# Kernel optimization log

Hardware: AMD Instinct MI355X
Metric: run time of the kernel (lower is better)

## Reference

```python
import jax, jax.numpy as jnp
import numpy as np

NUM_HEADS = 8

def setup_inputs() -> dict:
    key = jax.random.key(0)
    ks = jax.random.split(key, 5)
    b, c, h, w = 8, 512, 32, 32
    sd = 1.0 / np.sqrt(c)
    x = jax.random.normal(ks[0], (b, c, h, w), dtype=jnp.float32)
    Wq = jax.random.normal(ks[1], (c, c), dtype=jnp.float32) * sd
    Wk = jax.random.normal(ks[2], (c, c), dtype=jnp.float32) * sd
    Wv = jax.random.normal(ks[3], (c, c), dtype=jnp.float32) * sd
    Wo = jax.random.normal(ks[4], (c, c), dtype=jnp.float32) * sd
    z = jnp.zeros((c,), dtype=jnp.float32)
    return {"x": x, "Wq": Wq, "bq": z, "Wk": Wk, "bk": z, "Wv": Wv, "bv": z, "Wo": Wo, "bo": z}

def reference(x, Wq, bq, Wk, bk, Wv, bv, Wo, bo):
    b, c, h, w = x.shape
    nh = NUM_HEADS
    hd = c // nh
    # [b, c, h, w] -> [b, h*w, c]
    xr = jnp.transpose(x, (0, 2, 3, 1)).reshape(b, h * w, c)
    def proj(W, bias):
        y = xr @ W.T + bias
        return y.reshape(b, h * w, nh, hd)
    q = proj(Wq, bq)  # [b, s, nh, hd]
    k = proj(Wk, bk)
    v = proj(Wv, bv)
    scale = 1.0 / np.sqrt(hd)
    att = jnp.einsum("bsnd,btnd->bnst", q, k) * scale  # [b, nh, s, s]
    att = jax.nn.softmax(att, axis=-1)
    # dropout is identity in eval mode
    out = jnp.einsum("bnst,btnd->bsnd", att, v).reshape(b, h, w, c)
    out = out @ Wo.T + bo  # [b, h, w, c]
    return out
```

## Files before the change

### kernel.cpp

```cpp
#include <hip/hip_runtime.h>

typedef _Float16 half_t;
typedef _Float16 half2v __attribute__((ext_vector_type(2)));
typedef _Float16 half8 __attribute__((ext_vector_type(8)));
typedef float f32x4 __attribute__((ext_vector_type(4)));

static_assert(sizeof(half8) == 16, "half8 must be 16B");

__device__ inline half8 make_h8(unsigned long lo, unsigned long hi) {
  union { half8 v; unsigned long u[2]; } x;
  x.u[0] = lo; x.u[1] = hi;
  return x.v;
}

__device__ inline float fast_exp2(float x) {
#if __has_builtin(__builtin_amdgcn_exp2f)
  return __builtin_amdgcn_exp2f(x);
#else
  return exp2f(x);
#endif
}

__device__ inline half2v cvt_pk_f16(float lo, float hi) {
  return __builtin_bit_cast(half2v, __builtin_amdgcn_cvt_pkrtz(lo, hi));
}

__device__ inline void gload_lds16(const void* g, void* l) {
  __builtin_amdgcn_global_load_lds(
      (const __attribute__((address_space(1))) unsigned int*)g,
      (__attribute__((address_space(3))) unsigned int*)l, 16, 0, 0);
}

__global__ void prep_kernel(const float* __restrict__ x,
                            const float* __restrict__ w0, const float* __restrict__ w1,
                            const float* __restrict__ w2, const float* __restrict__ w3,
                            half_t* __restrict__ xr, half_t* __restrict__ wout) {
  if (blockIdx.z < 8) {
    __shared__ float t[32][33];
    const int b = blockIdx.z;
    const int c0 = blockIdx.y * 32;
    const int s0 = blockIdx.x * 32;
    const int tx = threadIdx.x, ty = threadIdx.y;
    const float* xp = x + ((size_t)b * 512 + c0) * 1024 + s0;
#pragma unroll
    for (int r = 0; r < 4; r++) {
      const int cl = ty + 8 * r;
      t[cl][tx] = xp[(size_t)cl * 1024 + tx];
    }
    __syncthreads();
    half_t* op = xr + ((size_t)b * 1024 + s0) * 512 + c0;
#pragma unroll
    for (int r = 0; r < 4; r++) {
      const int sl = ty + 8 * r;
      op[(size_t)sl * 512 + tx] = (half_t)t[tx][sl];
    }
  } else {
    const int f = blockIdx.x + 32 * blockIdx.y;
    const int tid = threadIdx.x + 32 * threadIdx.y;
    const int base = (f * 256 + tid) * 2;
#pragma unroll
    for (int r = 0; r < 2; r++) {
      const int i = base + r;
      const int mz = i >> 16;
      const float* src = (mz == 0) ? w0 : (mz == 1) ? w1 : (mz == 2) ? w2 : w3;
      const float4 v = ((const float4*)src)[i & 65535];
      union { half_t e[4]; unsigned long u; } st;
      st.e[0] = (half_t)v.x; st.e[1] = (half_t)v.y;
      st.e[2] = (half_t)v.z; st.e[3] = (half_t)v.w;
      *(unsigned long*)(wout + (size_t)i * 4) = st.u;
    }
  }
}

template <int MODE, int BM>
__global__ __launch_bounds__(256, 2) void gemm_kernel(
    const half_t* __restrict__ A, const half_t* __restrict__ Wall,
    const float* __restrict__ b0, const float* __restrict__ b1,
    const float* __restrict__ b2, half_t* __restrict__ qkv,
    float* __restrict__ fout) {
  constexpr int K = 512;
  constexpr int IREP = BM / 32;
  __shared__ alignas(16) half_t lA[BM * 64];
  __shared__ alignas(16) half_t lB[128 * 64];

  int bx, by, bz;
  {
    const int flat = blockIdx.x + gridDim.x * (blockIdx.y + gridDim.y * blockIdx.z);
    const int xcd = flat & 7;
    const int r = flat >> 3;
    if (MODE == 0) {
      bx = r & 3; bz = (r >> 2) % 3; by = (r / 12) * 8 + xcd;
    } else {
      bx = r & 3; bz = 0; by = (r >> 2) * 8 + xcd;
    }
  }

  const int z = bz;
  const half_t* W = Wall + (size_t)z * K * 512;
  const float* bias = (MODE == 1) ? b0 : (z == 0 ? b0 : (z == 1 ? b1 : b2));

  const int tid = threadIdx.x;
  const int lane = tid & 63;
  const int wid = tid >> 6;
  const int wm = wid >> 1, wn = wid & 1;
  const int g = lane >> 4, r16 = lane & 15;
  const int m0 = by * BM, n0 = bx * 128;

  f32x4 acc[IREP][4];
#pragma unroll
  for (int i = 0; i < IREP; i++)
#pragma unroll
    for (int j = 0; j < 4; j++) acc[i][j] = (f32x4){0.f, 0.f, 0.f, 0.f};

  for (int k0 = 0; k0 < K; k0 += 64) {
#pragma unroll
    for (int t = 0; t < BM / 32; t++) {
      const int o = (t * 256 + tid) * 16;
      const int row = o >> 7;
      const int kbs = (o & 127) ^ ((row & 7) << 4);
      gload_lds16((const char*)(A + (size_t)(m0 + row) * K + k0) + kbs, (char*)lA + o);
    }
#pragma unroll
    for (int t = 0; t < 4; t++) {
      const int o = (t * 256 + tid) * 16;
      const int row = o >> 7;
      const int kbs = (o & 127) ^ ((row & 7) << 4);
      gload_lds16((const char*)(W + (size_t)(n0 + row) * K + k0) + kbs, (char*)lB + o);
    }
    __syncthreads();
#pragma unroll
    for (int kk = 0; kk < 2; kk++) {
      half8 af[IREP], bf[4];
#pragma unroll
      for (int i = 0; i < IREP; i++) {
        const int row = wm * (BM / 2) + i * 16 + r16;
        const int sw = (row & 7) << 4;
        const char* p = (const char*)lA + row * 128;
        af[i] = make_h8(*(const unsigned long*)(p + ((kk * 64 + g * 8) ^ sw)),
                        *(const unsigned long*)(p + ((kk * 64 + 32 + g * 8) ^ sw)));
      }
#pragma unroll
      for (int j = 0; j < 4; j++) {
        const int row = wn * 64 + j * 16 + r16;
        const int sw = (row & 7) << 4;
        const char* p = (const char*)lB + row * 128;
        bf[j] = make_h8(*(const unsigned long*)(p + ((kk * 64 + g * 8) ^ sw)),
                        *(const unsigned long*)(p + ((kk * 64 + 32 + g * 8) ^ sw)));
      }
#pragma unroll
      for (int i = 0; i < IREP; i++)
#pragma unroll
        for (int j = 0; j < 4; j++)
          acc[i][j] = __builtin_amdgcn_mfma_f32_16x16x32_f16(af[i], bf[j], acc[i][j], 0, 0, 0);
    }
    __syncthreads();
  }

  half_t* dst = (MODE == 0) ? (qkv + (size_t)z * 4194304) : (half_t*)nullptr;
  const float scale = (MODE == 0 && z == 0) ? 0.18033688011112042f : 1.0f;
#pragma unroll
  for (int i = 0; i < IREP; i++) {
#pragma unroll
    for (int j = 0; j < 4; j++) {
      const int n = n0 + wn * 64 + j * 16 + r16;
      const float bvv = bias[n];
      const int mb = m0 + wm * (BM / 2) + i * 16 + g * 4;
      if (MODE == 0 && z == 2) {
        const int bb = mb >> 10, s0v = mb & 1023, hh = n >> 6, d = n & 63;
        const int kvb = s0v & 31;
        const int sp0 = (s0v & ~31) | ((((kvb & 15) >> 2) << 3) + ((kvb >> 4) << 2));
        half_t* dp = dst + (size_t)(bb * 8 + hh) * 65536 + ((size_t)d << 10) + sp0;
        union { half_t e[4]; unsigned long u; } st;
#pragma unroll
        for (int rr = 0; rr < 4; rr++) st.e[rr] = (half_t)(acc[i][j][rr] + bvv);
        *(unsigned long*)dp = st.u;
      } else {
#pragma unroll
        for (int rr = 0; rr < 4; rr++) {
          const int m = mb + rr;
          const float v = (acc[i][j][rr] + bvv) * scale;
          if (MODE == 0) {
            const int bb = m >> 10, s = m & 1023, hh = n >> 6, d = n & 63;
            dst[(((size_t)(bb * 8 + hh) * 1024 + s) << 6) + d] = (half_t)v;
          } else {
            fout[(size_t)m * 512 + n] = v;
          }
        }
      }
    }
  }
}


__device__ inline half8 lds_frag128(const half_t* l, int row, int cb) {
  const char* p = (const char*)l + row * 128 + (cb ^ ((row & 7) << 4));
  return *(const half8*)p;
}

__global__ __launch_bounds__(256) void attn_kernel(
    const half_t* __restrict__ Q, const half_t* __restrict__ Kh,
    const half_t* __restrict__ V, half_t* __restrict__ O) {
  __shared__ alignas(16) half_t lK[2][64 * 64];
  __shared__ alignas(16) half_t lV[2][64 * 64];

  const int tid = threadIdx.x;
  const int lane = tid & 63;
  const int w = tid >> 6;
  const int flat = blockIdx.x + (blockIdx.y << 3);
  const int xcd = flat & 7;
  const int tt = flat >> 3;
  const int qch = tt & 7;
  const int bh = ((tt >> 3) << 3) | xcd;
  const int b = bh >> 3, h = bh & 7;
  const int g = lane >> 4, r16 = lane & 15;
  const size_t base = (size_t)bh * 65536;
  const half_t* Qp = Q + base;
  const half_t* Kp = Kh + base;
  const half_t* Vt = V + base;
  const int q0 = qch * 128 + w * 32;

  half8 qf[2][2];
#pragma unroll
  for (int qt = 0; qt < 2; qt++) {
    const half_t* qrow = Qp + (size_t)(q0 + qt * 16 + r16) * 64 + g * 8;
    qf[qt][0] = *(const half8*)(qrow);
    qf[qt][1] = *(const half8*)(qrow + 32);
  }

  f32x4 acc[2][4];
#pragma unroll
  for (int qt = 0; qt < 2; qt++)
#pragma unroll
    for (int i = 0; i < 4; i++) acc[qt][i] = (f32x4){0.f, 0.f, 0.f, 0.f};
  float lsum[2] = {0.f, 0.f};

  auto stage = [&](int kv0, int bufi) {
    half_t* lk = lK[bufi];
    half_t* lv = lV[bufi];
    const char* ksrc = (const char*)(Kp + (size_t)kv0 * 64);
    const char* vsrc = (const char*)Vt + (size_t)kv0 * 2;
#pragma unroll
    for (int i = 0; i < 2; i++) {
      const int o = i * 4096 + tid * 16;
      const int row = o >> 7;
      const int cs = (o & 127) ^ ((row & 7) << 4);
      gload_lds16(ksrc + row * 128 + cs, (char*)lk + o);
      gload_lds16(vsrc + row * 2048 + cs, (char*)lv + o);
    }
  };

  stage(0, 0);
  __syncthreads();

  int buf = 0;
  for (int kv0 = 0; kv0 < 1024; kv0 += 64) {
    if (kv0 + 64 < 1024) stage(kv0 + 64, buf ^ 1);
    const half_t* lk = lK[buf];
    const half_t* lv = lV[buf];
#pragma unroll
    for (int sub = 0; sub < 2; sub++) {
      half8 kf0 = lds_frag128(lk, sub * 32 + r16, g * 16);
      half8 kf1 = lds_frag128(lk, sub * 32 + r16, 64 + g * 16);
      half8 kf2 = lds_frag128(lk, sub * 32 + 16 + r16, g * 16);
      half8 kf3 = lds_frag128(lk, sub * 32 + 16 + r16, 64 + g * 16);
      half8 vf[4];
#pragma unroll
      for (int dt = 0; dt < 4; dt++)
        vf[dt] = lds_frag128(lv, dt * 16 + r16, sub * 64 + g * 16);

#pragma unroll
      for (int qt = 0; qt < 2; qt++) {
        f32x4 s0 = {0.f, 0.f, 0.f, 0.f}, s1 = {0.f, 0.f, 0.f, 0.f};
        __builtin_amdgcn_s_setprio(1);
        s0 = __builtin_amdgcn_mfma_f32_16x16x32_f16(kf0, qf[qt][0], s0, 0, 0, 0);
        s0 = __builtin_amdgcn_mfma_f32_16x16x32_f16(kf1, qf[qt][1], s0, 0, 0, 0);
        s1 = __builtin_amdgcn_mfma_f32_16x16x32_f16(kf2, qf[qt][0], s1, 0, 0, 0);
        s1 = __builtin_amdgcn_mfma_f32_16x16x32_f16(kf3, qf[qt][1], s1, 0, 0, 0);
        __builtin_amdgcn_s_setprio(0);

        float p[8];
#pragma unroll
        for (int i = 0; i < 4; i++) { p[i] = fast_exp2(s0[i]); p[4 + i] = fast_exp2(s1[i]); }
        lsum[qt] += ((p[0] + p[1]) + (p[2] + p[3])) + ((p[4] + p[5]) + (p[6] + p[7]));

        union { half8 v; half2v h2[4]; } pu;
#pragma unroll
        for (int i = 0; i < 4; i++)
          pu.h2[i] = cvt_pk_f16(p[2 * i], p[2 * i + 1]);
        __builtin_amdgcn_s_setprio(1);
#pragma unroll
        for (int dt = 0; dt < 4; dt++)
          acc[qt][dt] = __builtin_amdgcn_mfma_f32_16x16x32_f16(vf[dt], pu.v, acc[qt][dt], 0, 0, 0);
        __builtin_amdgcn_s_setprio(0);
      }
    }
    __syncthreads();
    buf ^= 1;
  }

#pragma unroll
  for (int qt = 0; qt < 2; qt++) {
    float l = lsum[qt];
    l += __shfl_xor(l, 16);
    l += __shfl_xor(l, 32);
    const float inv = 1.f / l;
    half_t* orow = O + ((size_t)b * 1024 + q0 + qt * 16 + r16) * 512 + h * 64;
#pragma unroll
    for (int dt = 0; dt < 4; dt++) {
      union { half_t e[4]; unsigned long u; } st;
#pragma unroll
      for (int rr = 0; rr < 4; rr++) st.e[rr] = (half_t)(acc[qt][dt][rr] * inv);
      *(unsigned long*)(orow + dt * 16 + g * 4) = st.u;
    }
  }
}

extern "C" void kernel_launch(void* const* d_in, const int* in_sizes, int n_in,
                              void* d_out, int out_size, void* d_ws, size_t ws_size,
                              hipStream_t stream) {
  if (ws_size < 44040192u) return;
  const float* x  = (const float*)d_in[0];
  const float* Wq = (const float*)d_in[1];
  const float* bq = (const float*)d_in[2];
  const float* Wk = (const float*)d_in[3];
  const float* bk = (const float*)d_in[4];
  const float* Wv = (const float*)d_in[5];
  const float* bv = (const float*)d_in[6];
  const float* Wo = (const float*)d_in[7];
  const float* bo = (const float*)d_in[8];
  char* ws = (char*)d_ws;
  half_t* xr = (half_t*)(ws + 0);
  half_t* W4 = (half_t*)(ws + 8388608);
  half_t* Qb = (half_t*)(ws + 10485760);
  half_t* AO = (half_t*)(ws + 35651584);
  float* out = (float*)d_out;

  prep_kernel<<<dim3(32, 16, 9), dim3(32, 8), 0, stream>>>(x, Wq, Wk, Wv, Wo, xr, W4);
  gemm_kernel<0, 128><<<dim3(4, 64, 3), 256, 0, stream>>>(xr, W4, bq, bk, bv, Qb, nullptr);
  attn_kernel<<<dim3(8, 64), 256, 0, stream>>>(Qb, Qb + 4194304, Qb + 8388608, AO);
  gemm_kernel<1, 64><<<dim3(4, 128, 1), 256, 0, stream>>>(AO, W4 + 786432, bo, nullptr, nullptr,
                                                          nullptr, out);
}
```

Baseline: 70.55 us.

## Double KV tile to 128 and batch QK/PV MFMAs across query tiles

```diff
diff --git a/kernel.cpp b/kernel.cpp
--- a/kernel.cpp
+++ b/kernel.cpp
@@ -197,11 +197,16 @@
   return *(const half8*)p;
 }
 
+__device__ inline half8 lds_frag256(const half_t* l, int row, int cb) {
+  const char* p = (const char*)l + row * 256 + (cb ^ ((row & 7) << 4));
+  return *(const half8*)p;
+}
+
 __global__ __launch_bounds__(256) void attn_kernel(
     const half_t* __restrict__ Q, const half_t* __restrict__ Kh,
     const half_t* __restrict__ V, half_t* __restrict__ O) {
-  __shared__ alignas(16) half_t lK[2][64 * 64];
-  __shared__ alignas(16) half_t lV[2][64 * 64];
+  __shared__ alignas(16) half_t lK[2][128 * 64];
+  __shared__ alignas(16) half_t lV[2][64 * 128];
 
   const int tid = threadIdx.x;
   const int lane = tid & 63;
@@ -240,12 +245,14 @@
     const char* ksrc = (const char*)(Kp + (size_t)kv0 * 64);
     const char* vsrc = (const char*)Vt + (size_t)kv0 * 2;
 #pragma unroll
-    for (int i = 0; i < 2; i++) {
+    for (int i = 0; i < 4; i++) {
       const int o = i * 4096 + tid * 16;
-      const int row = o >> 7;
-      const int cs = (o & 127) ^ ((row & 7) << 4);
-      gload_lds16(ksrc + row * 128 + cs, (char*)lk + o);
-      gload_lds16(vsrc + row * 2048 + cs, (char*)lv + o);
+      const int krow = o >> 7;
+      const int kcs = (o & 127) ^ ((krow & 7) << 4);
+      gload_lds16(ksrc + krow * 128 + kcs, (char*)lk + o);
+      const int vrow = o >> 8;
+      const int vcs = (o & 255) ^ ((vrow & 7) << 4);
+      gload_lds16(vsrc + vrow * 2048 + vcs, (char*)lv + o);
     }
   };
 
@@ -253,12 +260,12 @@
   __syncthreads();
 
   int buf = 0;
-  for (int kv0 = 0; kv0 < 1024; kv0 += 64) {
-    if (kv0 + 64 < 1024) stage(kv0 + 64, buf ^ 1);
+  for (int kv0 = 0; kv0 < 1024; kv0 += 128) {
+    if (kv0 + 128 < 1024) stage(kv0 + 128, buf ^ 1);
     const half_t* lk = lK[buf];
     const half_t* lv = lV[buf];
 #pragma unroll
-    for (int sub = 0; sub < 2; sub++) {
+    for (int sub = 0; sub < 4; sub++) {
       half8 kf0 = lds_frag128(lk, sub * 32 + r16, g * 16);
       half8 kf1 = lds_frag128(lk, sub * 32 + r16, 64 + g * 16);
       half8 kf2 = lds_frag128(lk, sub * 32 + 16 + r16, g * 16);
@@ -266,33 +273,43 @@
       half8 vf[4];
 #pragma unroll
       for (int dt = 0; dt < 4; dt++)
-        vf[dt] = lds_frag128(lv, dt * 16 + r16, sub * 64 + g * 16);
-
+        vf[dt] = lds_frag256(lv, dt * 16 + r16, sub * 64 + g * 16);
+
+      f32x4 s[2][2];
+      __builtin_amdgcn_s_setprio(1);
 #pragma unroll
       for (int qt = 0; qt < 2; qt++) {
-        f32x4 s0 = {0.f, 0.f, 0.f, 0.f}, s1 = {0.f, 0.f, 0.f, 0.f};
-        __builtin_amdgcn_s_setprio(1);
-        s0 = __builtin_amdgcn_mfma_f32_16x16x32_f16(kf0, qf[qt][0], s0, 0, 0, 0);
-        s0 = __builtin_amdgcn_mfma_f32_16x16x32_f16(kf1, qf[qt][1], s0, 0, 0, 0);
-        s1 = __builtin_amdgcn_mfma_f32_16x16x32_f16(kf2, qf[qt][0], s1, 0, 0, 0);
-        s1 = __builtin_amdgcn_mfma_f32_16x16x32_f16(kf3, qf[qt][1], s1, 0, 0, 0);
-        __builtin_amdgcn_s_setprio(0);
-
+        s[qt][0] = (f32x4){0.f, 0.f, 0.f, 0.f};
+        s[qt][1] = (f32x4){0.f, 0.f, 0.f, 0.f};
+        s[qt][0] = __builtin_amdgcn_mfma_f32_16x16x32_f16(kf0, qf[qt][0], s[qt][0], 0, 0, 0);
+        s[qt][0] = __builtin_amdgcn_mfma_f32_16x16x32_f16(kf1, qf[qt][1], s[qt][0], 0, 0, 0);
+        s[qt][1] = __builtin_amdgcn_mfma_f32_16x16x32_f16(kf2, qf[qt][0], s[qt][1], 0, 0, 0);
+        s[qt][1] = __builtin_amdgcn_mfma_f32_16x16x32_f16(kf3, qf[qt][1], s[qt][1], 0, 0, 0);
+      }
+      __builtin_amdgcn_s_setprio(0);
+
+      union { half8 v; half2v h2[4]; } pu[2];
+#pragma unroll
+      for (int qt = 0; qt < 2; qt++) {
         float p[8];
 #pragma unroll
-        for (int i = 0; i < 4; i++) { p[i] = fast_exp2(s0[i]); p[4 + i] = fast_exp2(s1[i]); }
+        for (int i = 0; i < 4; i++) {
+          p[i] = fast_exp2(s[qt][0][i]);
+          p[4 + i] = fast_exp2(s[qt][1][i]);
+        }
         lsum[qt] += ((p[0] + p[1]) + (p[2] + p[3])) + ((p[4] + p[5]) + (p[6] + p[7]));
-
-        union { half8 v; half2v h2[4]; } pu;
 #pragma unroll
         for (int i = 0; i < 4; i++)
-          pu.h2[i] = cvt_pk_f16(p[2 * i], p[2 * i + 1]);
-        __builtin_amdgcn_s_setprio(1);
+          pu[qt].h2[i] = cvt_pk_f16(p[2 * i], p[2 * i + 1]);
+      }
+
+      __builtin_amdgcn_s_setprio(1);
+#pragma unroll
+      for (int qt = 0; qt < 2; qt++)
 #pragma unroll
         for (int dt = 0; dt < 4; dt++)
-          acc[qt][dt] = __builtin_amdgcn_mfma_f32_16x16x32_f16(vf[dt], pu.v, acc[qt][dt], 0, 0, 0);
-        __builtin_amdgcn_s_setprio(0);
-      }
+          acc[qt][dt] = __builtin_amdgcn_mfma_f32_16x16x32_f16(vf[dt], pu[qt].v, acc[qt][dt], 0, 0, 0);
+      __builtin_amdgcn_s_setprio(0);
     }
     __syncthreads();
     buf ^= 1;
```

After: 70.51 us. No clear change (-0.1%).
